# Kernel optimization log

Measured on AMD Instinct MI355X. Metric: run time of the kernel, lower is better.

## Reference

```python
import jax, jax.numpy as jnp
import numpy as np

GRID_SIZE = 5
SPLINE_ORDER = 3
GRID_MIN = -1.0
GRID_MAX = 1.0
H = (GRID_MAX - GRID_MIN) / GRID_SIZE          # grid interval
G0 = GRID_MIN - SPLINE_ORDER * H               # first (extended) knot = grid[:,0]


def _basis_matrix():
    # Uniform B-spline power-basis matrix, same recurrence as the torch code.
    M = np.array([[1.0]], dtype=np.float64)
    scalar = 1.0
    for k in range(2, SPLINE_ORDER + 2):
        t1 = np.pad(M, ((0, 1), (0, 0)))
        t3 = np.pad(M, ((1, 0), (0, 0)))
        t2 = np.zeros((k - 1, k))
        t4 = np.zeros((k - 1, k))
        for i in range(k - 1):
            t2[i, i] = i + 1
            t2[i, i + 1] = k - (i + 2)
            t4[i, i] = -1.0
            t4[i, i + 1] = 1.0
        M = t1 @ t2 + t3 @ t4
        scalar *= 1.0 / (k - 1)
    return (M * scalar).astype(np.float32)

BASIS = jnp.asarray(_basis_matrix())  # (spline_order+1, spline_order+1)


def setup_inputs():
    key = jax.random.key(0)
    k1, k2, k3 = jax.random.split(key, 3)
    N, FIN, FOUT = 2048, 128, 128
    x = jax.random.normal(k1, (N, FIN), dtype=jnp.float32)
    base_weight = jax.random.normal(k2, (FOUT, FIN), dtype=jnp.float32) * 0.1
    spline_weight = jax.random.normal(k3, (FIN, FOUT, GRID_SIZE + SPLINE_ORDER), dtype=jnp.float32) * 0.1
    return {"x": x, "base_weight": base_weight, "spline_weight": spline_weight}


def _forward(x, base_weight, spline_weight):
    N, fin = x.shape
    fout = base_weight.shape[0]
    k = SPLINE_ORDER
    # base branch: SiLU activation then linear
    base_out = jax.nn.silu(x) @ base_weight.T                       # (N, fout)
    # input normalization: Hardtanh around grid center (shift=0, scale=1 for [-1,1])
    shift = (GRID_MIN + GRID_MAX) / 2.0
    scale = (GRID_MAX - GRID_MIN) / 2.0
    xn = jnp.clip((x - shift) / scale, -1.0, 1.0) * scale + shift
    # bucketize: bin index + fractional position (replaces floor/compare + torch.nonzero)
    t = (xn - G0) / H
    fl = jnp.floor(t)
    u1 = t - fl                                                     # (x - interval_floor) / interval
    idx = jnp.clip(fl.astype(jnp.int32), k, k + GRID_SIZE - 1)      # clamped knot-interval index
    cfloor = idx - k                                                # (N, fin) first control point index
    # power bases [1, u, u^2, ..., u^k] -> b-spline basis via basis matrix
    pows = u1[..., None] ** jnp.arange(k + 1, dtype=x.dtype)        # (N, fin, k+1)
    bspl = pows @ BASIS.astype(x.dtype)                             # (N, fin, k+1)
    # faithful to torch: spline_weight.view(out, in, -1) memory reinterpretation
    cp = jnp.reshape(spline_weight, (fout, fin, GRID_SIZE + k))
    gidx = cfloor[..., None] + jnp.arange(k + 1)                    # (N, fin, k+1) control point indices
    i_idx = jnp.arange(fin)[None, :, None]
    gathered = cp[:, i_idx, gidx]                                   # (fout, N, fin, k+1)
    gathered = jnp.transpose(gathered, (1, 0, 2, 3))                # (N, fout, fin, k+1)
    # faithful to torch: .view(N, in, k+1, out) memory reinterpretation
    cpr = jnp.reshape(gathered, (N, fin, k + 1, fout))
    # per-feature spline matmul then sum over in_features (KAN aggregation)
    spline_out = jnp.einsum('nij,nijo->no', bspl, cpr)              # (N, fout)
    return base_out + spline_out


def reference(x, base_weight, spline_weight):
    return _forward(x, base_weight, spline_weight)
```

## Files before the change

kernel.cpp:

```cpp
#include <hip/hip_runtime.h>
#include <hip/hip_bf16.h>
#include <math.h>

typedef __attribute__((ext_vector_type(8))) short short8;
typedef __attribute__((ext_vector_type(4))) float floatx4;

typedef unsigned int uint_a   __attribute__((may_alias));
typedef uint2        uint2_a  __attribute__((may_alias));
typedef uint4        uint4_a  __attribute__((may_alias));
typedef short8       short8_a __attribute__((may_alias));

static __device__ __forceinline__ unsigned short bfbits(float f) {
    __hip_bfloat16 h = __float2bfloat16(f);
    unsigned short u;
    __builtin_memcpy(&u, &h, 2);
    return u;
}
static __device__ __forceinline__ unsigned pack2(float lo, float hi) {
    return (unsigned)bfbits(lo) | ((unsigned)bfbits(hi) << 16);
}

#define SP_STR  136
#define SBN_STR 68
#define ST_STR  68
#define STB_STR 36
#define SC_STR  132

__global__ __launch_bounds__(256, 2) void kan_fused(
    const float* __restrict__ x,
    const float* __restrict__ bw,
    const float* __restrict__ sw,
    float* __restrict__ out)
{
    __shared__ short sP[5 * 16 * SP_STR];
    __shared__ short sBn[4 * 64 * SBN_STR];
    __shared__ float sT[4 * 16 * ST_STR];
    __shared__ float sTb[16 * STB_STR];
    __shared__ unsigned char sC[16 * SC_STR];

    const int tid = threadIdx.x;
    const int nb  = blockIdx.x >> 2;
    const int s   = blockIdx.x & 3;
    const int n0  = nb * 16;

    const int w = tid >> 6, l = tid & 63;
    const int m = l & 15, q = l >> 4;

    const int r  = tid >> 4;
    const int i0 = (tid & 15) * 8;
    float v[8];
    *(float4*)(v)     = *(const float4*)(x + (n0 + r) * 128 + i0);
    *(float4*)(v + 4) = *(const float4*)(x + (n0 + r) * 128 + i0 + 4);

    const int cc = s + 4 * w;
    const float* swp = sw + cc * 64 + m * 4;
    float4 pre[16];
#pragma unroll
    for (int rr = 0; rr < 16; ++rr)
        pre[rr] = *(const float4*)(swp + (q + 4 * rr) * 1024);

    float4 bw8[8];
    if (w >= 2) {
        const float* bwp = bw + (32 * s + 16 * (w - 2) + m) * 128 + q * 8;
#pragma unroll
        for (int kk = 0; kk < 4; ++kk) {
            bw8[2 * kk]     = *(const float4*)(bwp + kk * 32);
            bw8[2 * kk + 1] = *(const float4*)(bwp + kk * 32 + 4);
        }
    }

    {
        float A5[5][8];
        unsigned char cc8[8];
#pragma unroll
        for (int i = 0; i < 8; ++i) {
            float xv = v[i];
            float si = xv / (1.0f + expf(-xv));
            float xn = fminf(fmaxf(xv, -1.0f), 1.0f);
            float t  = (xn + 2.2f) / 0.4f;
            float u  = t - floorf(t);
            int idx  = (int)floorf(t);
            idx = min(max(idx, 3), 7);
            cc8[i] = (unsigned char)(idx - 3);
            float u2 = u * u, u3 = u2 * u, om = 1.0f - u;
            A5[0][i] = om * om * om * (1.0f / 6.0f);
            A5[1][i] = 0.5f * u3 - u2 + (2.0f / 3.0f);
            A5[2][i] = -0.5f * u3 + 0.5f * u2 + 0.5f * u + (1.0f / 6.0f);
            A5[3][i] = u3 * (1.0f / 6.0f);
            A5[4][i] = si;
        }
#pragma unroll
        for (int g = 0; g < 5; ++g) {
            unsigned p0 = pack2(A5[g][0], A5[g][1]);
            unsigned p1 = pack2(A5[g][2], A5[g][3]);
            unsigned p2 = pack2(A5[g][4], A5[g][5]);
            unsigned p3 = pack2(A5[g][6], A5[g][7]);
            *(uint4_a*)(&sP[(g * 16 + r) * SP_STR + i0]) = make_uint4(p0, p1, p2, p3);
        }
        *(uint_a*)(&sC[r * SC_STR + i0])     = cc8[0] | (cc8[1]<<8) | (cc8[2]<<16) | (cc8[3]<<24);
        *(uint_a*)(&sC[r * SC_STR + i0 + 4]) = cc8[4] | (cc8[5]<<8) | (cc8[6]<<16) | (cc8[7]<<24);
    }

#pragma unroll
    for (int rr = 0; rr < 16; ++rr)
        *(uint2_a*)(&sBn[(w * 64 + q + 4 * rr) * SBN_STR + m * 4]) =
            make_uint2(pack2(pre[rr].x, pre[rr].y), pack2(pre[rr].z, pre[rr].w));

    __syncthreads();

    float4 pre2[16];
#pragma unroll
    for (int rr = 0; rr < 16; ++rr)
        pre2[rr] = *(const float4*)(swp + (64 + q + 4 * rr) * 1024);

    const short* tile = &sBn[w * 64 * SBN_STR];
    const short* ap   = &sP[(w * 16 + m) * SP_STR + q * 8];
    floatx4 acc[4] = {{0.f,0.f,0.f,0.f},{0.f,0.f,0.f,0.f},
                      {0.f,0.f,0.f,0.f},{0.f,0.f,0.f,0.f}};

#pragma unroll
    for (int kh = 0; kh < 2; ++kh) {
        short8 af = *(const short8_a*)(ap + kh * 32);
#pragma unroll
        for (int cg = 0; cg < 4; ++cg) {
            short8 bf;
#pragma unroll
            for (int j2 = 0; j2 < 8; ++j2)
                bf[j2] = tile[(kh * 32 + q * 8 + j2) * SBN_STR + cg * 16 + m];
            acc[cg] = __builtin_amdgcn_mfma_f32_16x16x32_bf16(af, bf, acc[cg], 0, 0, 0);
        }
    }

#pragma unroll
    for (int rr = 0; rr < 16; ++rr)
        *(uint2_a*)(&sBn[(w * 64 + q + 4 * rr) * SBN_STR + m * 4]) =
            make_uint2(pack2(pre2[rr].x, pre2[rr].y), pack2(pre2[rr].z, pre2[rr].w));

#pragma unroll
    for (int kh = 0; kh < 2; ++kh) {
        short8 af = *(const short8_a*)(ap + (2 + kh) * 32);
#pragma unroll
        for (int cg = 0; cg < 4; ++cg) {
            short8 bf;
#pragma unroll
            for (int j2 = 0; j2 < 8; ++j2)
                bf[j2] = tile[(kh * 32 + q * 8 + j2) * SBN_STR + cg * 16 + m];
            acc[cg] = __builtin_amdgcn_mfma_f32_16x16x32_bf16(af, bf, acc[cg], 0, 0, 0);
        }
    }

#pragma unroll
    for (int cg = 0; cg < 4; ++cg)
#pragma unroll
        for (int rr = 0; rr < 4; ++rr)
            sT[(w * 16 + q * 4 + rr) * ST_STR + cg * 16 + m] = acc[cg][rr];

    if (w >= 2) {
        const short* ap4 = &sP[(4 * 16 + m) * SP_STR + q * 8];
        floatx4 ab = {0.f, 0.f, 0.f, 0.f};
#pragma unroll
        for (int kk = 0; kk < 4; ++kk) {
            short8 af = *(const short8_a*)(ap4 + kk * 32);
            uint4 pb = make_uint4(pack2(bw8[2*kk].x,   bw8[2*kk].y),
                                  pack2(bw8[2*kk].z,   bw8[2*kk].w),
                                  pack2(bw8[2*kk+1].x, bw8[2*kk+1].y),
                                  pack2(bw8[2*kk+1].z, bw8[2*kk+1].w));
            short8 bf;
            __builtin_memcpy(&bf, &pb, 16);
            ab = __builtin_amdgcn_mfma_f32_16x16x32_bf16(af, bf, ab, 0, 0, 0);
        }
#pragma unroll
        for (int rr = 0; rr < 4; ++rr)
            sTb[(q * 4 + rr) * STB_STR + 16 * (w - 2) + m] = ab[rr];
    }

    __syncthreads();

    const int gn = tid >> 4, go2 = tid & 15;
    const int oh = 8 * s + (go2 >> 1);
    float racc0 = sTb[gn * STB_STR + 2 * go2];
    float racc1 = sTb[gn * STB_STR + 2 * go2 + 1];
#pragma unroll
    for (int j = 0; j < 4; ++j) {
        int c   = sC[gn * SC_STR + 32 * j + oh];
        int rel = 8 * (go2 >> 1) + c + 2 * (go2 & 1);
        racc0 += sT[(j * 16 + gn) * ST_STR + rel];
        racc1 += sT[(j * 16 + gn) * ST_STR + rel + 1];
    }
    *(float2*)(out + (n0 + gn) * 128 + 32 * s + 2 * go2) = make_float2(racc0, racc1);
}

extern "C" void kernel_launch(void* const* d_in, const int* in_sizes, int n_in,
                              void* d_out, int out_size, void* d_ws, size_t ws_size,
                              hipStream_t stream) {
    const float* x  = (const float*)d_in[0];
    const float* bw = (const float*)d_in[1];
    const float* sw = (const float*)d_in[2];
    float* out = (float*)d_out;
    kan_fused<<<dim3(512), dim3(256), 0, stream>>>(x, bw, sw, out);
}
```

Before: 63.19 us.

## Feed spline weights directly from global into MFMA operands, drop LDS staging

Spline-weight fragments are now loaded straight from global memory into registers in MFMA operand layout and double-buffered across the four K steps, with A and B operands swapped. This removes the LDS staging buffer sBn, its writes and its strided scalar LDS reads, and also lets accumulator results go to LDS as float4 stores. In exchange, the global loads become scalar and strided (16 lanes contiguous per row), which may weaken coalescing and raise register pressure.

```diff
diff --git a/kernel.cpp b/kernel.cpp
--- a/kernel.cpp
+++ b/kernel.cpp
@@ -6,7 +6,6 @@
 typedef __attribute__((ext_vector_type(4))) float floatx4;
 
 typedef unsigned int uint_a   __attribute__((may_alias));
-typedef uint2        uint2_a  __attribute__((may_alias));
 typedef uint4        uint4_a  __attribute__((may_alias));
 typedef short8       short8_a __attribute__((may_alias));
 
@@ -21,7 +20,6 @@
 }
 
 #define SP_STR  136
-#define SBN_STR 68
 #define ST_STR  68
 #define STB_STR 36
 #define SC_STR  132
@@ -33,7 +31,6 @@
     float* __restrict__ out)
 {
     __shared__ short sP[5 * 16 * SP_STR];
-    __shared__ short sBn[4 * 64 * SBN_STR];
     __shared__ float sT[4 * 16 * ST_STR];
     __shared__ float sTb[16 * STB_STR];
     __shared__ unsigned char sC[16 * SC_STR];
@@ -53,11 +50,14 @@
     *(float4*)(v + 4) = *(const float4*)(x + (n0 + r) * 128 + i0 + 4);
 
     const int cc = s + 4 * w;
-    const float* swp = sw + cc * 64 + m * 4;
-    float4 pre[16];
+    const float* gA = sw + cc * 64 + q * 8 * 1024 + m;
+
+    float f[2][4][8];
 #pragma unroll
-    for (int rr = 0; rr < 16; ++rr)
-        pre[rr] = *(const float4*)(swp + (q + 4 * rr) * 1024);
+    for (int cg = 0; cg < 4; ++cg)
+#pragma unroll
+        for (int j2 = 0; j2 < 8; ++j2)
+            f[0][cg][j2] = gA[j2 * 1024 + cg * 16];
 
     float4 bw8[8];
     if (w >= 2) {
@@ -101,59 +101,39 @@
         *(uint_a*)(&sC[r * SC_STR + i0 + 4]) = cc8[4] | (cc8[5]<<8) | (cc8[6]<<16) | (cc8[7]<<24);
     }
 
-#pragma unroll
-    for (int rr = 0; rr < 16; ++rr)
-        *(uint2_a*)(&sBn[(w * 64 + q + 4 * rr) * SBN_STR + m * 4]) =
-            make_uint2(pack2(pre[rr].x, pre[rr].y), pack2(pre[rr].z, pre[rr].w));
-
     __syncthreads();
 
-    float4 pre2[16];
-#pragma unroll
-    for (int rr = 0; rr < 16; ++rr)
-        pre2[rr] = *(const float4*)(swp + (64 + q + 4 * rr) * 1024);
-
-    const short* tile = &sBn[w * 64 * SBN_STR];
-    const short* ap   = &sP[(w * 16 + m) * SP_STR + q * 8];
     floatx4 acc[4] = {{0.f,0.f,0.f,0.f},{0.f,0.f,0.f,0.f},
                       {0.f,0.f,0.f,0.f},{0.f,0.f,0.f,0.f}};
+    const short* bp = &sP[(w * 16 + m) * SP_STR + q * 8];
 
 #pragma unroll
-    for (int kh = 0; kh < 2; ++kh) {
-        short8 af = *(const short8_a*)(ap + kh * 32);
+    for (int kh = 0; kh < 4; ++kh) {
+        if (kh < 3) {
+#pragma unroll
+            for (int cg = 0; cg < 4; ++cg)
+#pragma unroll
+                for (int j2 = 0; j2 < 8; ++j2)
+                    f[(kh + 1) & 1][cg][j2] = gA[((kh + 1) * 32 + j2) * 1024 + cg * 16];
+        }
+        short8 bf = *(const short8_a*)(bp + kh * 32);
 #pragma unroll
         for (int cg = 0; cg < 4; ++cg) {
-            short8 bf;
-#pragma unroll
-            for (int j2 = 0; j2 < 8; ++j2)
-                bf[j2] = tile[(kh * 32 + q * 8 + j2) * SBN_STR + cg * 16 + m];
+            uint4 pa = make_uint4(pack2(f[kh & 1][cg][0], f[kh & 1][cg][1]),
+                                  pack2(f[kh & 1][cg][2], f[kh & 1][cg][3]),
+                                  pack2(f[kh & 1][cg][4], f[kh & 1][cg][5]),
+                                  pack2(f[kh & 1][cg][6], f[kh & 1][cg][7]));
+            short8 af;
+            __builtin_memcpy(&af, &pa, 16);
             acc[cg] = __builtin_amdgcn_mfma_f32_16x16x32_bf16(af, bf, acc[cg], 0, 0, 0);
         }
     }
 
 #pragma unroll
-    for (int rr = 0; rr < 16; ++rr)
-        *(uint2_a*)(&sBn[(w * 64 + q + 4 * rr) * SBN_STR + m * 4]) =
-            make_uint2(pack2(pre2[rr].x, pre2[rr].y), pack2(pre2[rr].z, pre2[rr].w));
-
-#pragma unroll
-    for (int kh = 0; kh < 2; ++kh) {
-        short8 af = *(const short8_a*)(ap + (2 + kh) * 32);
-#pragma unroll
-        for (int cg = 0; cg < 4; ++cg) {
-            short8 bf;
-#pragma unroll
-            for (int j2 = 0; j2 < 8; ++j2)
-                bf[j2] = tile[(kh * 32 + q * 8 + j2) * SBN_STR + cg * 16 + m];
-            acc[cg] = __builtin_amdgcn_mfma_f32_16x16x32_bf16(af, bf, acc[cg], 0, 0, 0);
-        }
+    for (int cg = 0; cg < 4; ++cg) {
+        float4 st = make_float4(acc[cg][0], acc[cg][1], acc[cg][2], acc[cg][3]);
+        *(float4*)(&sT[(w * 16 + m) * ST_STR + cg * 16 + q * 4]) = st;
     }
-
-#pragma unroll
-    for (int cg = 0; cg < 4; ++cg)
-#pragma unroll
-        for (int rr = 0; rr < 4; ++rr)
-            sT[(w * 16 + q * 4 + rr) * ST_STR + cg * 16 + m] = acc[cg][rr];
 
     if (w >= 2) {
         const short* ap4 = &sP[(4 * 16 + m) * SP_STR + q * 8];
```

Measured after the change: 64.07 us. About the same (+1.4%).
